# Kernel optimization log

Hardware: AMD Instinct MI355X
Metric: run time of the kernel (lower is better)

The kernel has to match this reference:

```python
import jax, jax.numpy as jnp
import numpy as np

N_NODES = 15000
N_EDGES = 60000
D_NODE_IN = 74
D_EDGE_IN = 12
D = 64            # node_out_feats
D_EHID = 128      # edge_hidden_feats
N_STEPS = 6
BN_EPS = 1e-5


def setup_inputs() -> dict:
    key = jax.random.key(0)
    ks = jax.random.split(key, 16)
    def lin(k, fan_in, shape):
        return jax.random.normal(k, shape, jnp.float32) / np.sqrt(fan_in)
    inp = {
        "node_feats": jax.random.normal(ks[0], (N_NODES, D_NODE_IN), jnp.float32),
        "edge_feats": jax.random.normal(ks[1], (N_EDGES, D_EDGE_IN), jnp.float32),
        "src": jax.random.randint(ks[2], (N_EDGES,), 0, N_NODES, jnp.int32),
        "dst": jax.random.randint(ks[3], (N_EDGES,), 0, N_NODES, jnp.int32),
        # project_node_feats: Linear(node_in, D)
        "W_proj": lin(ks[4], D_NODE_IN, (D_NODE_IN, D)),
        "b_proj": jnp.zeros((D,), jnp.float32),
        # edge network: Linear(edge_in, ehid) -> ReLU -> Linear(ehid, D*D)
        "W_e1": lin(ks[5], D_EDGE_IN, (D_EDGE_IN, D_EHID)),
        "b_e1": jnp.zeros((D_EHID,), jnp.float32),
        "W_e2": lin(ks[6], D_EHID, (D_EHID, D * D)),
        "b_e2": jnp.zeros((D * D,), jnp.float32),
        # NNConv bias + BatchNorm affine params
        "conv_bias": jnp.zeros((D,), jnp.float32),
        "bn_gamma": jnp.ones((D,), jnp.float32),
        "bn_beta": jnp.zeros((D,), jnp.float32),
        # GRU (single layer): torch layout W_ih [3D, D], W_hh [3D, D]
        "W_ih": lin(ks[7], D, (3 * D, D)),
        "W_hh": lin(ks[8], D, (3 * D, D)),
        "b_ih": jnp.zeros((3 * D,), jnp.float32),
        "b_hh": jnp.zeros((3 * D,), jnp.float32),
    }
    return inp


def reference(node_feats, edge_feats, W_proj, b_proj, W_e1, b_e1, W_e2, b_e2,
              conv_bias, bn_gamma, bn_beta, W_ih, W_hh, b_ih, b_hh, src, dst):
    n_nodes = node_feats.shape[0]

    # project_node_feats: Linear + ReLU
    h = jax.nn.relu(node_feats @ W_proj + b_proj)          # [N, D]
    hidden = h                                              # GRU hidden state

    # edge MLP is a pure function of static edge_feats -> compute once
    ew = jax.nn.relu(edge_feats @ W_e1 + b_e1) @ W_e2 + b_e2
    ew = ew.reshape(-1, D, D)                               # [E, D, D]

    # mean-aggregation normalizer (DGL mean: 0 for isolated nodes)
    deg = jax.ops.segment_sum(jnp.ones_like(dst, jnp.float32), dst,
                              num_segments=n_nodes)
    inv_deg = jnp.where(deg > 0, 1.0 / jnp.maximum(deg, 1.0), 0.0)[:, None]

    for _ in range(N_STEPS):
        # per-edge matvec message: (h_src^T W_e); sum over d_in commutes
        # with the mean reduction, so reduce vectors instead of matrices.
        msg = jnp.einsum('ei,eio->eo', h[src], ew)          # [E, D]
        rst = jax.ops.segment_sum(msg, dst, num_segments=n_nodes) * inv_deg
        rst = rst + conv_bias
        # BatchNorm1d (training mode: batch statistics, biased variance)
        mu = rst.mean(axis=0)
        var = rst.var(axis=0)
        rst = (rst - mu) * jax.lax.rsqrt(var + BN_EPS) * bn_gamma + bn_beta
        m = jax.nn.relu(rst)
        # GRU cell (torch gate order: r, z, n)
        gi = m @ W_ih.T + b_ih
        gh = hidden @ W_hh.T + b_hh
        i_r, i_z, i_n = jnp.split(gi, 3, axis=-1)
        h_r, h_z, h_n = jnp.split(gh, 3, axis=-1)
        r = jax.nn.sigmoid(i_r + h_r)
        z = jax.nn.sigmoid(i_z + h_z)
        n = jnp.tanh(i_n + r * h_n)
        hidden = (1.0 - z) * n + z * hidden
        h = hidden
    return h
```

## Files before the change

### kernel.cpp

```cpp
#include <hip/hip_runtime.h>
#include <hip/hip_bf16.h>
#include <math.h>

#define NN 15000
#define NE 60000
#define DIN 74
#define DEIN 12
#define DD 64
#define EH 128
#define NG 8192
#define NSTEPS 6
#define NRB 235
#define KAB 384
#define NTMAX 18752
#define NFB 586

typedef unsigned short ushort_t;
typedef __attribute__((ext_vector_type(8))) short short8v;
typedef __attribute__((ext_vector_type(4))) float float4v;

__device__ __forceinline__ float bsf(unsigned short u){
  union { unsigned int i; float f; } v; v.i = ((unsigned int)u) << 16; return v.f;
}
__device__ __forceinline__ unsigned short fsb(float f){
  union { float f; unsigned int i; } v; v.f = f;
  unsigned int x = v.i;
  return (unsigned short)((x + 0x7FFFu + ((x >> 16) & 1u)) >> 16);
}
__device__ __forceinline__ unsigned int pkbf(float a, float b){
  __hip_bfloat162 r = __float22bfloat162_rn(make_float2(a, b));
  union { __hip_bfloat162 h; unsigned int u; } v; v.h = r; return v.u;
}

__global__ void k_sniff(const ushort_t* __restrict__ nf16,
                        const int* __restrict__ dsti, int* __restrict__ flags){
  __shared__ int cnt[2];
  int t = threadIdx.x;
  if (t < 2) cnt[t] = 0;
  __syncthreads();
  int bad = 0;
  for (int i = t; i < 1024; i += 256){
    unsigned short u = nf16[2*i];
    int e = (u >> 7) & 0xFF;
    if (e < 96 || e > 159) bad++;
  }
  if (bad) atomicAdd(&cnt[0], bad);
  if (t < 256 && dsti[2*t+1] == 0) atomicAdd(&cnt[1], 1);
  __syncthreads();
  if (t == 0){
    flags[0] = (cnt[0] > 300) ? 1 : 0;
    flags[1] = (cnt[1] > 250) ? 1 : 0;
  }
}

struct CanonArgs {
  const void* in[15];
  float* out[15];
  int n[15];
};
__global__ void k_canon_all(CanonArgs a, const int* __restrict__ flags){
  int j = blockIdx.y;
  int n = a.n[j];
  int fp32 = flags[0];
  const void* in = a.in[j];
  float* out = a.out[j];
  for (int i = blockIdx.x*256 + threadIdx.x; i < n; i += gridDim.x*256){
    if (fp32) out[i] = ((const float*)in)[i];
    else      out[i] = bsf(((const ushort_t*)in)[i]);
  }
}
__global__ void k_canoni(const void* __restrict__ in, int* __restrict__ out,
                         int n, const int* __restrict__ flags){
  int i = blockIdx.x*256 + threadIdx.x;
  if (i >= n) return;
  long long v = flags[1] ? ((const long long*)in)[i]
                         : (long long)((const int*)in)[i];
  int vi = (int)v;
  if (vi < 0) vi = 0;
  if (vi >= NN) vi = NN-1;
  out[i] = vi;
}

__global__ void k_proj(const float* __restrict__ nf, const float* __restrict__ Wp,
                       const float* __restrict__ bp, float* __restrict__ hid,
                       ushort_t* __restrict__ ab){
  __shared__ float nfl[4][DIN];
  int t = threadIdx.x, blk = blockIdx.x;
  for (int idx = t; idx < 4*DIN; idx += 256){
    int vl = idx / DIN, i = idx - vl*DIN;
    nfl[vl][i] = nf[(size_t)(blk*4+vl)*DIN + i];
  }
  __syncthreads();
  int vl = t >> 6, o = t & 63;
  int v = blk*4 + vl;
  float acc = bp[o];
  for (int i = 0; i < DIN; ++i) acc += nfl[vl][i] * Wp[i*DD + o];
  float r = fmaxf(acc, 0.f);
  hid[(size_t)v*DD + o] = r;
  ushort_t hh = fsb(r);
  float hl = r - bsf(hh);
  ab[(size_t)v*KAB + 64 + o]  = hh;
  ab[(size_t)v*KAB + 192 + o] = fsb(hl);
  ab[(size_t)v*KAB + 320 + o] = hh;
}

__global__ void k_emlp(const float* __restrict__ ef, const float* __restrict__ W1,
                       const float* __restrict__ b1, ushort_t* __restrict__ thi,
                       ushort_t* __restrict__ tlo){
  __shared__ float efl[2][DEIN];
  int t = threadIdx.x, blk = blockIdx.x;
  if (t < 2*DEIN){
    int el = t / DEIN, i = t - el*DEIN;
    efl[el][i] = ef[(size_t)(blk*2+el)*DEIN + i];
  }
  __syncthreads();
  int el = t >> 7, c = t & 127;
  float acc = b1[c];
  for (int i = 0; i < DEIN; ++i) acc += efl[el][i] * W1[i*EH + c];
  float tv = fmaxf(acc, 0.f);
  ushort_t hiv = fsb(tv);
  size_t off = (size_t)(blk*2+el)*EH + c;
  thi[off] = hiv;
  tlo[off] = fsb(tv - bsf(hiv));
}
__global__ void k_zpad(ushort_t* __restrict__ thi, ushort_t* __restrict__ tlo){
  int t = threadIdx.x;
  thi[(size_t)NE*EH + t] = 0;
  tlo[(size_t)NE*EH + t] = 0;
}

__global__ void k_w2q(const float* __restrict__ W2, const float* __restrict__ b2,
                      ushort_t* __restrict__ w2q, ushort_t* __restrict__ w2b){
  int idx = blockIdx.x*256 + threadIdx.x;
  if (idx < NG*DD){
    int n = idx >> 6, i = idx & 63;
    int kq = n >> 11, rem = n & 2047;
    int o = rem >> 5, kl = rem & 31;
    int kg = kq*32 + kl;
    w2q[idx] = fsb(W2[(size_t)kg*4096 + i*64 + o]);
  } else if (idx < NG*DD + DD*DD){
    int r = idx - NG*DD;
    int o = r >> 6, i = r & 63;
    w2b[r] = fsb(b2[i*64 + o]);
  }
}

__global__ void k_wgru(const float* __restrict__ Wih, const float* __restrict__ Whh,
                       ushort_t* __restrict__ wg){
  int pos = blockIdx.x*256 + threadIdx.x;
  if (pos >= 256*KAB) return;
  int c = pos / KAB, k = pos - c*KAB;
  int kb = k >> 6, i = k & 63;
  int g = c >> 6, o = c & 63;
  float w = 0.f;
  if ((kb & 1) == 0){
    if (g == 0)      w = Wih[(size_t)(o)*64 + i];
    else if (g == 1) w = Wih[(size_t)(64+o)*64 + i];
    else if (g == 2) w = Wih[(size_t)(128+o)*64 + i];
  } else {
    if (g == 0)      w = Whh[(size_t)(o)*64 + i];
    else if (g == 1) w = Whh[(size_t)(64+o)*64 + i];
    else if (g == 3) w = Whh[(size_t)(128+o)*64 + i];
  }
  ushort_t hi = fsb(w);
  wg[pos] = (kb >= 4) ? fsb(w - bsf(hi)) : hi;
}

__global__ void k_zero(int* __restrict__ p, int n){
  int i = blockIdx.x*256 + threadIdx.x;
  if (i < n) p[i] = 0;
}
__global__ void k_deg(const int* __restrict__ idxarr, int* __restrict__ deg){
  int e = blockIdx.x*256 + threadIdx.x;
  if (e < NE) atomicAdd(&deg[idxarr[e]], 1);
}
__global__ void k_scan(const int* __restrict__ deg, int* __restrict__ rowp,
                       float* __restrict__ invd){
  __shared__ int ssum[256];
  int t = threadIdx.x;
  const int STRIP = (NN + 255) / 256;
  int lo = t*STRIP, hi = (lo + STRIP < NN) ? lo + STRIP : NN;
  int s = 0;
  for (int i = lo; i < hi; ++i) s += deg[i];
  ssum[t] = s;
  __syncthreads();
  if (t == 0){
    int acc = 0;
    for (int i = 0; i < 256; ++i){ int v = ssum[i]; ssum[i] = acc; acc += v; }
  }
  __syncthreads();
  int acc = ssum[t];
  for (int i = lo; i < hi; ++i){
    rowp[i] = acc;
    int d = deg[i];
    invd[i] = (d > 0) ? 1.0f/(float)d : 0.0f;
    acc += d;
  }
  if (t == 255) rowp[NN] = acc;
}
__global__ void k_scatter(const int* __restrict__ idxarr, const int* __restrict__ rowp,
                          int* __restrict__ cursor, int* __restrict__ eidx,
                          int* __restrict__ epos){
  int e = blockIdx.x*256 + threadIdx.x;
  if (e < NE){
    int d = idxarr[e];
    int pos = atomicAdd(&cursor[d], 1);
    int slot = rowp[d] + pos;
    eidx[slot] = e;
    if (epos) epos[e] = slot;
  }
}

__global__ void k_tiles(const int* __restrict__ rowp, int* __restrict__ tnode,
                        int* __restrict__ tbase, int* __restrict__ tcnt,
                        int* __restrict__ ntb){
  __shared__ int ss[256];
  int t = threadIdx.x;
  const int STRIP = (NN + 255) / 256;
  int lo = t*STRIP, hi = lo + STRIP; if (hi > NN) hi = NN;
  int c = 0;
  for (int i = lo; i < hi; ++i){
    int deg = rowp[i+1] - rowp[i];
    c += (deg + 15) >> 4;
  }
  ss[t] = c;
  __syncthreads();
  if (t == 0){
    int a = 0;
    for (int i = 0; i < 256; ++i){ int v = ss[i]; ss[i] = a; a += v; }
    ntb[0] = a;
  }
  __syncthreads();
  int pos = ss[t];
  for (int i = lo; i < hi; ++i){
    int b = rowp[i], deg = rowp[i+1] - b;
    for (int r = 0; r < deg; r += 16){
      tnode[pos] = i; tbase[pos] = b + r;
      int c2 = deg - r; tcnt[pos] = (c2 > 16) ? 16 : c2;
      ++pos;
    }
  }
}

__global__ __launch_bounds__(512,4) void k_fused6(
    const ushort_t* __restrict__ ab, const ushort_t* __restrict__ w2q,
    const ushort_t* __restrict__ w2b, const ushort_t* __restrict__ thi,
    const ushort_t* __restrict__ tlo,
    const int* __restrict__ tnode, const int* __restrict__ tbase,
    const int* __restrict__ tcnt, const int* __restrict__ ntb,
    const int* __restrict__ eidx, const int* __restrict__ epos,
    float* __restrict__ msg){
  __shared__ __align__(16) ushort_t Gl[32768];
  __shared__ float bhl[32*66];
  __shared__ int nodl[32], cntl[32], basel[32];
  __shared__ int eidl[32][16];
  __shared__ int posl[32][16];

  int tid = threadIdx.x;
  int nt = ntb[0];
  int T0 = blockIdx.x * 32;
  if (T0 >= nt) return;
  int wv = tid >> 6, lane = tid & 63;
  int lr = lane & 15, quad = lane >> 4;

  if (tid < 32){
    int gt = T0 + tid;
    int node = 0, base = 0, cnt = 0;
    if (gt < nt){ node = tnode[gt]; base = tbase[gt]; cnt = tcnt[gt]; }
    nodl[tid] = node; basel[tid] = base; cntl[tid] = cnt;
  }
  __syncthreads();
  {
    int j = tid >> 4, sl = tid & 15;
    int eid = NE, ps = 0;
    if (sl < cntl[j]){
      eid = eidx[basel[j] + sl];
      ps = epos[eid];
    }
    eidl[j][sl] = eid;
    posl[j][sl] = ps;
  }
  short8v hf0k0, hf0k1, hf1k0, hf1k1;
  {
    int n0 = nodl[lr], n1 = nodl[16 + lr];
    hf0k0 = *(const short8v*)(ab + (size_t)n0*KAB + 64 + quad*8);
    hf0k1 = *(const short8v*)(ab + (size_t)n0*KAB + 96 + quad*8);
    hf1k0 = *(const short8v*)(ab + (size_t)n1*KAB + 64 + quad*8);
    hf1k1 = *(const short8v*)(ab + (size_t)n1*KAB + 96 + quad*8);
  }
  {
    int ot = wv & 3, mh = wv >> 2;
    float4v ba = (float4v){0.f,0.f,0.f,0.f};
    short8v a0 = *(const short8v*)(w2b + (size_t)(ot*16 + lr)*DD + quad*8);
    short8v a1 = *(const short8v*)(w2b + (size_t)(ot*16 + lr)*DD + 32 + quad*8);
    ba = __builtin_amdgcn_mfma_f32_16x16x32_bf16(a0, mh ? hf1k0 : hf0k0, ba, 0,0,0);
    ba = __builtin_amdgcn_mfma_f32_16x16x32_bf16(a1, mh ? hf1k1 : hf0k1, ba, 0,0,0);
    #pragma unroll
    for (int reg = 0; reg < 4; ++reg)
      bhl[(mh*16 + lr)*66 + ot*16 + quad*4 + reg] = ba[reg];
  }

  int j0 = wv*4;
  for (int oh = 0; oh < 2; ++oh){
    float4v acc[4][2];
    #pragma unroll
    for (int j = 0; j < 4; ++j)
      #pragma unroll
      for (int ot = 0; ot < 2; ++ot)
        acc[j][ot] = (float4v){0.f,0.f,0.f,0.f};
    for (int kq = 0; kq < 4; ++kq){
      __syncthreads();
      short8v th0, th1, th2, th3, tw0, tw1, tw2, tw3;
      {
        size_t kqo = (size_t)kq*32 + quad*8;
        int e0 = eidl[j0+0][lr], e1 = eidl[j0+1][lr];
        int e2 = eidl[j0+2][lr], e3 = eidl[j0+3][lr];
        th0 = *(const short8v*)(thi + (size_t)e0*EH + kqo);
        tw0 = *(const short8v*)(tlo + (size_t)e0*EH + kqo);
        th1 = *(const short8v*)(thi + (size_t)e1*EH + kqo);
        tw1 = *(const short8v*)(tlo + (size_t)e1*EH + kqo);
        th2 = *(const short8v*)(thi + (size_t)e2*EH + kqo);
        tw2 = *(const short8v*)(tlo + (size_t)e2*EH + kqo);
        th3 = *(const short8v*)(thi + (size_t)e3*EH + kqo);
        tw3 = *(const short8v*)(tlo + (size_t)e3*EH + kqo);
      }
      #pragma unroll 2
      for (int it = 0; it < 8; ++it){
        int tile = wv*8 + it;
        int nrow = kq*2048 + oh*1024 + tile*16 + lr;
        const ushort_t* arow = w2q + (size_t)nrow*DD;
        short8v a0 = *(const short8v*)(arow + quad*8);
        short8v a1 = *(const short8v*)(arow + 32 + quad*8);
        int ol = tile >> 1;
        int klb = ((tile & 1) << 4) + quad*4;
        int q8 = klb >> 3, jj = klb & 7;
        #pragma unroll
        for (int mh = 0; mh < 2; ++mh){
          float4v g = (float4v){0.f,0.f,0.f,0.f};
          g = __builtin_amdgcn_mfma_f32_16x16x32_bf16(a0, mh ? hf1k0 : hf0k0, g, 0,0,0);
          g = __builtin_amdgcn_mfma_f32_16x16x32_bf16(a1, mh ? hf1k1 : hf0k1, g, 0,0,0);
          int m = mh*16 + lr;
          unsigned int p0 = pkbf(g[0], g[1]);
          unsigned int p1 = pkbf(g[2], g[3]);
          int byt = ((((m*4 + q8)*32 + ol) << 4) + jj*2) ^ ((m & 7) << 4);
          uint2 pv; pv.x = p0; pv.y = p1;
          *(uint2*)((char*)Gl + byt) = pv;
        }
      }
      __syncthreads();
      #pragma unroll
      for (int j = 0; j < 4; ++j){
        int m = j0 + j;
        int swz = (m & 7) << 4;
        short8v thj = (j==0)?th0:(j==1)?th1:(j==2)?th2:th3;
        short8v twj = (j==0)?tw0:(j==1)?tw1:(j==2)?tw2:tw3;
        #pragma unroll
        for (int ot = 0; ot < 2; ++ot){
          int byt = (((m*4 + quad)*32 + ot*16 + lr) << 4) ^ swz;
          short8v gf = *(const short8v*)((const char*)Gl + byt);
          acc[j][ot] = __builtin_amdgcn_mfma_f32_16x16x32_bf16(thj, gf, acc[j][ot], 0,0,0);
          acc[j][ot] = __builtin_amdgcn_mfma_f32_16x16x32_bf16(twj, gf, acc[j][ot], 0,0,0);
        }
      }
    }
    #pragma unroll
    for (int j = 0; j < 4; ++j){
      int m = j0 + j;
      #pragma unroll
      for (int ot = 0; ot < 2; ++ot){
        int o = oh*32 + ot*16 + lr;
        float bb = bhl[m*66 + o];
        #pragma unroll
        for (int reg = 0; reg < 4; ++reg){
          int sl = quad*4 + reg;
          int eid = eidl[m][sl];
          if (eid < NE) msg[(size_t)posl[m][sl]*DD + o] = acc[j][ot][reg] + bb;
        }
      }
    }
  }
}

__global__ void k_red(const float* __restrict__ msg, const int* __restrict__ rowp_d,
                      const float* __restrict__ invd, const float* __restrict__ cbias,
                      float* __restrict__ rst, float* __restrict__ part,
                      int* __restrict__ cnt, float* __restrict__ stats){
  __shared__ float ls[256], ls2[256];
  __shared__ int lastflag;
  int t = threadIdx.x, blk = blockIdx.x;
  int o = t & 63, gg = t >> 6;
  float cb = cbias[o];
  float s = 0.f, s2 = 0.f;
  #pragma unroll 1
  for (int j = 0; j < 16; ++j){
    int n = blk*64 + gg*16 + j;
    if (n >= NN) break;
    int b = rowp_d[n], e = rowp_d[n+1];
    float a0 = 0.f, a1 = 0.f, a2 = 0.f, a3 = 0.f;
    int i = b;
    for (; i + 3 < e; i += 4){
      a0 += msg[(size_t)i*DD + o];
      a1 += msg[(size_t)(i+1)*DD + o];
      a2 += msg[(size_t)(i+2)*DD + o];
      a3 += msg[(size_t)(i+3)*DD + o];
    }
    for (; i < e; ++i) a0 += msg[(size_t)i*DD + o];
    float x = ((a0 + a1) + (a2 + a3)) * invd[n] + cb;
    rst[(size_t)n*DD + o] = x;
    s += x; s2 += x*x;
  }
  ls[t] = s; ls2[t] = s2;
  __syncthreads();
  if (gg == 0){
    part[blk*128 + o]      = ls[o] + ls[64+o] + ls[128+o] + ls[192+o];
    part[blk*128 + 64 + o] = ls2[o] + ls2[64+o] + ls2[128+o] + ls2[192+o];
  }
  __threadfence();
  __syncthreads();
  if (t == 0) lastflag = (atomicAdd(cnt, 1) == NRB - 1) ? 1 : 0;
  __syncthreads();
  if (lastflag){
    if (t < 128){
      float s0 = 0.f, s1 = 0.f, s2b = 0.f, s3 = 0.f;
      int b = 0;
      for (; b + 3 < NRB; b += 4){
        s0  += part[b*128 + t];
        s1  += part[(b+1)*128 + t];
        s2b += part[(b+2)*128 + t];
        s3  += part[(b+3)*128 + t];
      }
      for (; b < NRB; ++b) s0 += part[b*128 + t];
      ls[t] = (s0 + s1) + (s2b + s3);
    }
    __syncthreads();
    if (t < 64){
      float mu = ls[t] / (float)NN;
      float var = ls[64+t] / (float)NN - mu*mu;
      if (var < 0.f) var = 0.f;
      stats[t] = mu;
      stats[64 + t] = rsqrtf(var + 1e-5f);
    }
  }
}

__global__ void k_gru_pre(const float* __restrict__ rst, const float* __restrict__ stats,
      const float* __restrict__ gamma, const float* __restrict__ beta,
      ushort_t* __restrict__ ab){
  int t = threadIdx.x, blk = blockIdx.x;
  int vl = t >> 6, o = t & 63;
  int v = blk*4 + vl;
  float x = rst[(size_t)v*DD + o];
  float m = fmaxf((x - stats[o])*stats[64+o]*gamma[o] + beta[o], 0.f);
  ushort_t mh = fsb(m);
  float mlo = m - bsf(mh);
  ab[(size_t)v*KAB + o]       = mh;
  ab[(size_t)v*KAB + 128 + o] = fsb(mlo);
  ab[(size_t)v*KAB + 256 + o] = mh;
}

__global__ __launch_bounds__(256) void k_gru_gemm(const ushort_t* __restrict__ ab,
        const ushort_t* __restrict__ wg, float* __restrict__ gbuf){
  __shared__ __align__(16) ushort_t As[128][136];
  __shared__ __align__(16) ushort_t Bs[64][136];
  int t = threadIdx.x;
  int n0 = blockIdx.x * 64;
  int m0 = blockIdx.y * 128;
  int w = t >> 6, lane = t & 63;
  int lrow = lane & 15, quad = lane >> 4;
  float4v acc[2][4];
  #pragma unroll
  for (int mt = 0; mt < 2; ++mt)
    #pragma unroll
    for (int nt = 0; nt < 4; ++nt) acc[mt][nt] = (float4v){0.f,0.f,0.f,0.f};
  for (int kt = 0; kt < 3; ++kt){
    __syncthreads();
    #pragma unroll
    for (int it = 0; it < 8; ++it){
      int cid = t + it*256;
      int r = cid >> 4, ko = (cid & 15) * 8;
      int gm = m0 + r; if (gm >= NN) gm = NN-1;
      *(uint4*)&As[r][ko] = *(const uint4*)(ab + (size_t)gm*KAB + kt*128 + ko);
    }
    #pragma unroll
    for (int it = 0; it < 4; ++it){
      int cid = t + it*256;
      int r = cid >> 4, ko = (cid & 15) * 8;
      *(uint4*)&Bs[r][ko] = *(const uint4*)(wg + (size_t)(n0 + r)*KAB + kt*128 + ko);
    }
    __syncthreads();
    #pragma unroll
    for (int ks = 0; ks < 4; ++ks){
      short8v a0 = *(const short8v*)&As[w*32 + lrow][ks*32 + quad*8];
      short8v a1 = *(const short8v*)&As[w*32 + 16 + lrow][ks*32 + quad*8];
      #pragma unroll
      for (int nt = 0; nt < 4; ++nt){
        short8v b = *(const short8v*)&Bs[nt*16 + lrow][ks*32 + quad*8];
        acc[0][nt] = __builtin_amdgcn_mfma_f32_16x16x32_bf16(a0, b, acc[0][nt], 0, 0, 0);
        acc[1][nt] = __builtin_amdgcn_mfma_f32_16x16x32_bf16(a1, b, acc[1][nt], 0, 0, 0);
      }
    }
  }
  #pragma unroll
  for (int mt = 0; mt < 2; ++mt){
    #pragma unroll
    for (int nt = 0; nt < 4; ++nt){
      int col = n0 + nt*16 + lrow;
      #pragma unroll
      for (int reg = 0; reg < 4; ++reg){
        int m = m0 + w*32 + mt*16 + quad*4 + reg;
        if (m < NN) gbuf[(size_t)m*256 + col] = acc[mt][nt][reg];
      }
    }
  }
}

__global__ void k_gru_fin(const float* __restrict__ gbuf,
      const float* __restrict__ bih, const float* __restrict__ bhh,
      float* __restrict__ hid, ushort_t* __restrict__ ab,
      float* __restrict__ out, int write_out){
  int t = threadIdx.x, blk = blockIdx.x;
  int vl = t >> 6, o = t & 63;
  int v = blk*4 + vl;
  const float* gb = gbuf + (size_t)v*256;
  float aR  = gb[o]       + bih[o]      + bhh[o];
  float aZ  = gb[64 + o]  + bih[64+o]   + bhh[64+o];
  float aNi = gb[128 + o] + bih[128+o];
  float aNh = gb[192 + o] + bhh[128+o];
  float hprev = hid[(size_t)v*DD + o];
  float r = 1.f/(1.f+__expf(-aR));
  float z = 1.f/(1.f+__expf(-aZ));
  float n = tanhf(aNi + r*aNh);
  float hnew = (1.f - z)*n + z*hprev;
  hid[(size_t)v*DD + o] = hnew;
  ushort_t hh = fsb(hnew);
  float hl = hnew - bsf(hh);
  ab[(size_t)v*KAB + 64 + o]  = hh;
  ab[(size_t)v*KAB + 192 + o] = fsb(hl);
  ab[(size_t)v*KAB + 320 + o] = hh;
  if (write_out) out[(size_t)v*DD + o] = hnew;
}

extern "C" void kernel_launch(void* const* d_in, const int* in_sizes, int n_in,
                              void* d_out, int out_size, void* d_ws, size_t ws_size,
                              hipStream_t stream){
  (void)out_size; (void)ws_size;
  float* out = (float*)d_out;

  int p_nf=-1,p_ef=-1,p_src=-1,p_dst=-1,p_Wp=-1,p_bp=-1,p_W1=-1,p_b1=-1,
      p_W2=-1,p_b2=-1,p_cb=-1,p_gam=-1,p_bet=-1,p_Wih=-1,p_Whh=-1,p_bih=-1,p_bhh=-1;
  int c60000=0,c64=0,c12288=0,c192=0;
  for (int i = 0; i < n_in; ++i){
    switch (in_sizes[i]){
      case 1110000: p_nf = i; break;
      case 720000:  p_ef = i; break;
      case 60000:   if (c60000++ == 0) p_src = i; else p_dst = i; break;
      case 4736:    p_Wp = i; break;
      case 64:      { if (c64==0) p_bp=i; else if (c64==1) p_cb=i;
                      else if (c64==2) p_gam=i; else p_bet=i; c64++; } break;
      case 1536:    p_W1 = i; break;
      case 128:     p_b1 = i; break;
      case 524288:  p_W2 = i; break;
      case 4096:    p_b2 = i; break;
      case 12288:   if (c12288++ == 0) p_Wih = i; else p_Whh = i; break;
      case 192:    if (c192++ == 0) p_bih = i; else p_bhh = i; break;
      default: break;
    }
  }

  char* p = (char*)d_ws;
  auto alloc = [&](size_t bytes)->char*{
    char* r = p; p += (bytes + 255) & ~(size_t)255; return r;
  };
  int* flags = (int*)alloc(256);
  const int FPOS[15] = {p_nf,p_ef,p_Wp,p_bp,p_W1,p_b1,p_W2,p_b2,p_cb,p_gam,p_bet,
                        p_Wih,p_Whh,p_bih,p_bhh};
  CanonArgs ca;
  int maxn = 0;
  for (int j = 0; j < 15; ++j){
    int n = in_sizes[FPOS[j]];
    ca.in[j]  = d_in[FPOS[j]];
    ca.out[j] = (float*)alloc((size_t)n * 4);
    ca.n[j]   = n;
    if (n > maxn) maxn = n;
  }
  const float* nf  = ca.out[0];  const float* ef  = ca.out[1];
  const float* Wp  = ca.out[2];  const float* bp  = ca.out[3];
  const float* W1  = ca.out[4];  const float* b1  = ca.out[5];
  const float* W2  = ca.out[6];  const float* b2  = ca.out[7];
  const float* cb  = ca.out[8];  const float* gam = ca.out[9];
  const float* bet = ca.out[10]; const float* Wih = ca.out[11];
  const float* Whh = ca.out[12]; const float* bih = ca.out[13];
  const float* bhh = ca.out[14];
  int* srcc = (int*)alloc((size_t)NE*4);
  int* dstc = (int*)alloc((size_t)NE*4);

  ushort_t* thi   = (ushort_t*)alloc((size_t)(NE+1)*EH*2);
  ushort_t* tlo   = (ushort_t*)alloc((size_t)(NE+1)*EH*2);
  ushort_t* w2q   = (ushort_t*)alloc((size_t)NG*DD*2);
  ushort_t* w2b   = (ushort_t*)alloc((size_t)DD*DD*2);
  float* hid      = (float*)alloc((size_t)NN*DD*4);
  ushort_t* ab    = (ushort_t*)alloc((size_t)NN*KAB*2);
  ushort_t* wg    = (ushort_t*)alloc((size_t)256*KAB*2);
  float* gbuf     = (float*)alloc((size_t)NN*256*4);
  float* rst      = (float*)alloc((size_t)NN*DD*4);
  float* msg      = (float*)alloc((size_t)NE*DD*4);
  float* part     = (float*)alloc((size_t)NRB*128*4);
  float* stats    = (float*)alloc(128*4);
  int* degall     = (int*)alloc((size_t)4*NN*4);
  int* deg  = degall;
  int* curd = degall + NN;
  int* deg2 = degall + 2*NN; int* cursor2 = degall + 3*NN;
  float* invd = (float*)alloc((size_t)NN*4);
  int* rowp_d = (int*)alloc((size_t)(NN+1)*4);
  int* eidx_d = (int*)alloc((size_t)NE*4);
  int* epos   = (int*)alloc((size_t)NE*4);
  int* rowp2  = (int*)alloc((size_t)(NN+1)*4);
  float* invd2= (float*)alloc((size_t)NN*4);
  int* eidx2  = (int*)alloc((size_t)NE*4);
  int* tnode  = (int*)alloc((size_t)NTMAX*4);
  int* tbase  = (int*)alloc((size_t)NTMAX*4);
  int* tcnt   = (int*)alloc((size_t)NTMAX*4);
  int* ntb    = (int*)alloc(256);
  int* cnts   = (int*)alloc(256);

  k_sniff<<<1, 256, 0, stream>>>((const ushort_t*)d_in[p_nf], (const int*)d_in[p_dst], flags);
  k_canon_all<<<dim3((maxn+255)/256, 15), 256, 0, stream>>>(ca, flags);
  k_canoni<<<(NE+255)/256, 256, 0, stream>>>(d_in[p_src], srcc, NE, flags);
  k_canoni<<<(NE+255)/256, 256, 0, stream>>>(d_in[p_dst], dstc, NE, flags);

  k_proj <<<NN/4,  256, 0, stream>>>(nf, Wp, bp, hid, ab);
  k_emlp <<<NE/2,  256, 0, stream>>>(ef, W1, b1, thi, tlo);
  k_zpad <<<1, 128, 0, stream>>>(thi, tlo);
  k_w2q  <<<(NG*DD + DD*DD + 255)/256, 256, 0, stream>>>(W2, b2, w2q, w2b);
  k_wgru <<<(256*KAB+255)/256, 256, 0, stream>>>(Wih, Whh, wg);
  k_zero <<<(4*NN+255)/256, 256, 0, stream>>>(degall, 4*NN);
  k_zero <<<1, 64, 0, stream>>>(cnts, 64);
  k_deg  <<<(NE+255)/256, 256, 0, stream>>>(dstc, deg);
  k_deg  <<<(NE+255)/256, 256, 0, stream>>>(srcc, deg2);
  k_scan <<<1, 256, 0, stream>>>(deg,  rowp_d, invd);
  k_scan <<<1, 256, 0, stream>>>(deg2, rowp2, invd2);
  k_scatter<<<(NE+255)/256, 256, 0, stream>>>(dstc, rowp_d, curd, eidx_d, epos);
  k_scatter<<<(NE+255)/256, 256, 0, stream>>>(srcc, rowp2, cursor2, eidx2, (int*)0);
  k_tiles<<<1, 256, 0, stream>>>(rowp2, tnode, tbase, tcnt, ntb);

  for (int s = 0; s < NSTEPS; ++s){
    k_fused6<<<NFB, 512, 0, stream>>>(ab, w2q, w2b, thi, tlo,
                                      tnode, tbase, tcnt, ntb, eidx2, epos, msg);
    k_red <<<NRB, 256, 0, stream>>>(msg, rowp_d, invd, cb, rst, part,
                                    cnts + s, stats);
    k_gru_pre <<<NN/4, 256, 0, stream>>>(rst, stats, gam, bet, ab);
    k_gru_gemm<<<dim3(4, (NN+127)/128), 256, 0, stream>>>(ab, wg, gbuf);
    k_gru_fin <<<NN/4, 256, 0, stream>>>(gbuf, bih, bhh, hid, ab, out,
                                         (s == NSTEPS-1) ? 1 : 0);
  }
}
```

Before: 1.162 ms.

## Fuse BN-apply, GRU GEMM and GRU gates into one kernel per step

Replaces the per-step k_gru_pre, k_gru_gemm and k_gru_fin kernels with a single k_gru_one kernel. It applies batch-norm and ReLU while loading tiles, runs the 256-wide gate GEMM, and computes the GRU gates from LDS, which removes the gbuf global round trip and two launches. Batch-norm statistics now come from a separate single-block k_bnf kernel instead of the last-block atomic pattern, and it pre-folds gamma and beta into a scale and shift. The message kernel also moves its edge-feature gathers after the G-tile compute and raises the unroll factor, to hide that load latency. In exchange the fused GRU kernel needs about 150KB of LDS, which limits it to one block per CU, and the ab columns 0–63 are no longer refreshed.

```diff
diff --git a/kernel.cpp b/kernel.cpp
--- a/kernel.cpp
+++ b/kernel.cpp
@@ -11,6 +11,7 @@
 #define NG 8192
 #define NSTEPS 6
 #define NRB 235
+#define NGB 235
 #define KAB 384
 #define NTMAX 18752
 #define NFB 586
@@ -242,7 +243,7 @@
   }
 }
 
-__global__ __launch_bounds__(512,4) void k_fused6(
+__global__ __launch_bounds__(512,4) void k_fused7(
     const ushort_t* __restrict__ ab, const ushort_t* __restrict__ w2q,
     const ushort_t* __restrict__ w2b, const ushort_t* __restrict__ thi,
     const ushort_t* __restrict__ tlo,
@@ -310,21 +311,7 @@
         acc[j][ot] = (float4v){0.f,0.f,0.f,0.f};
     for (int kq = 0; kq < 4; ++kq){
       __syncthreads();
-      short8v th0, th1, th2, th3, tw0, tw1, tw2, tw3;
-      {
-        size_t kqo = (size_t)kq*32 + quad*8;
-        int e0 = eidl[j0+0][lr], e1 = eidl[j0+1][lr];
-        int e2 = eidl[j0+2][lr], e3 = eidl[j0+3][lr];
-        th0 = *(const short8v*)(thi + (size_t)e0*EH + kqo);
-        tw0 = *(const short8v*)(tlo + (size_t)e0*EH + kqo);
-        th1 = *(const short8v*)(thi + (size_t)e1*EH + kqo);
-        tw1 = *(const short8v*)(tlo + (size_t)e1*EH + kqo);
-        th2 = *(const short8v*)(thi + (size_t)e2*EH + kqo);
-        tw2 = *(const short8v*)(tlo + (size_t)e2*EH + kqo);
-        th3 = *(const short8v*)(thi + (size_t)e3*EH + kqo);
-        tw3 = *(const short8v*)(tlo + (size_t)e3*EH + kqo);
-      }
-      #pragma unroll 2
+      #pragma unroll 4
       for (int it = 0; it < 8; ++it){
         int tile = wv*8 + it;
         int nrow = kq*2048 + oh*1024 + tile*16 + lr;
@@ -347,6 +334,20 @@
           *(uint2*)((char*)Gl + byt) = pv;
         }
       }
+      short8v th0, th1, th2, th3, tw0, tw1, tw2, tw3;
+      {
+        size_t kqo = (size_t)kq*32 + quad*8;
+        int e0 = eidl[j0+0][lr], e1 = eidl[j0+1][lr];
+        int e2 = eidl[j0+2][lr], e3 = eidl[j0+3][lr];
+        th0 = *(const short8v*)(thi + (size_t)e0*EH + kqo);
+        tw0 = *(const short8v*)(tlo + (size_t)e0*EH + kqo);
+        th1 = *(const short8v*)(thi + (size_t)e1*EH + kqo);
+        tw1 = *(const short8v*)(tlo + (size_t)e1*EH + kqo);
+        th2 = *(const short8v*)(thi + (size_t)e2*EH + kqo);
+        tw2 = *(const short8v*)(tlo + (size_t)e2*EH + kqo);
+        th3 = *(const short8v*)(thi + (size_t)e3*EH + kqo);
+        tw3 = *(const short8v*)(tlo + (size_t)e3*EH + kqo);
+      }
       __syncthreads();
       #pragma unroll
       for (int j = 0; j < 4; ++j){
@@ -383,10 +384,8 @@
 
 __global__ void k_red(const float* __restrict__ msg, const int* __restrict__ rowp_d,
                       const float* __restrict__ invd, const float* __restrict__ cbias,
-                      float* __restrict__ rst, float* __restrict__ part,
-                      int* __restrict__ cnt, float* __restrict__ stats){
+                      float* __restrict__ rst, float* __restrict__ part){
   __shared__ float ls[256], ls2[256];
-  __shared__ int lastflag;
   int t = threadIdx.x, blk = blockIdx.x;
   int o = t & 63, gg = t >> 6;
   float cb = cbias[o];
@@ -415,129 +414,131 @@
     part[blk*128 + o]      = ls[o] + ls[64+o] + ls[128+o] + ls[192+o];
     part[blk*128 + 64 + o] = ls2[o] + ls2[64+o] + ls2[128+o] + ls2[192+o];
   }
-  __threadfence();
-  __syncthreads();
-  if (t == 0) lastflag = (atomicAdd(cnt, 1) == NRB - 1) ? 1 : 0;
-  __syncthreads();
-  if (lastflag){
-    if (t < 128){
-      float s0 = 0.f, s1 = 0.f, s2b = 0.f, s3 = 0.f;
-      int b = 0;
-      for (; b + 3 < NRB; b += 4){
-        s0  += part[b*128 + t];
-        s1  += part[(b+1)*128 + t];
-        s2b += part[(b+2)*128 + t];
-        s3  += part[(b+3)*128 + t];
-      }
-      for (; b < NRB; ++b) s0 += part[b*128 + t];
-      ls[t] = (s0 + s1) + (s2b + s3);
-    }
-    __syncthreads();
-    if (t < 64){
-      float mu = ls[t] / (float)NN;
-      float var = ls[64+t] / (float)NN - mu*mu;
-      if (var < 0.f) var = 0.f;
-      stats[t] = mu;
-      stats[64 + t] = rsqrtf(var + 1e-5f);
-    }
-  }
-}
-
-__global__ void k_gru_pre(const float* __restrict__ rst, const float* __restrict__ stats,
-      const float* __restrict__ gamma, const float* __restrict__ beta,
-      ushort_t* __restrict__ ab){
-  int t = threadIdx.x, blk = blockIdx.x;
-  int vl = t >> 6, o = t & 63;
-  int v = blk*4 + vl;
-  float x = rst[(size_t)v*DD + o];
-  float m = fmaxf((x - stats[o])*stats[64+o]*gamma[o] + beta[o], 0.f);
-  ushort_t mh = fsb(m);
-  float mlo = m - bsf(mh);
-  ab[(size_t)v*KAB + o]       = mh;
-  ab[(size_t)v*KAB + 128 + o] = fsb(mlo);
-  ab[(size_t)v*KAB + 256 + o] = mh;
-}
-
-__global__ __launch_bounds__(256) void k_gru_gemm(const ushort_t* __restrict__ ab,
-        const ushort_t* __restrict__ wg, float* __restrict__ gbuf){
-  __shared__ __align__(16) ushort_t As[128][136];
-  __shared__ __align__(16) ushort_t Bs[64][136];
+}
+
+__global__ void k_bnf(const float* __restrict__ part, const float* __restrict__ gamma,
+                      const float* __restrict__ beta, float* __restrict__ stats){
+  __shared__ float sh[128];
   int t = threadIdx.x;
-  int n0 = blockIdx.x * 64;
-  int m0 = blockIdx.y * 128;
-  int w = t >> 6, lane = t & 63;
-  int lrow = lane & 15, quad = lane >> 4;
-  float4v acc[2][4];
+  float s0 = 0.f, s1 = 0.f, s2 = 0.f, s3 = 0.f;
+  int b = 0;
+  for (; b + 3 < NRB; b += 4){
+    s0 += part[b*128 + t];
+    s1 += part[(b+1)*128 + t];
+    s2 += part[(b+2)*128 + t];
+    s3 += part[(b+3)*128 + t];
+  }
+  for (; b < NRB; ++b) s0 += part[b*128 + t];
+  sh[t] = (s0 + s1) + (s2 + s3);
+  __syncthreads();
+  if (t < 64){
+    float mu = sh[t] / (float)NN;
+    float var = sh[64+t] / (float)NN - mu*mu;
+    if (var < 0.f) var = 0.f;
+    float rsq = rsqrtf(var + 1e-5f);
+    float scl = rsq * gamma[t];
+    stats[t] = scl;
+    stats[64 + t] = beta[t] - mu*scl;
+  }
+}
+
+__global__ __launch_bounds__(512) void k_gru_one(
+    const float* __restrict__ rst, const float* __restrict__ stats,
+    ushort_t* __restrict__ ab, const ushort_t* __restrict__ wg,
+    const float* __restrict__ bih, const float* __restrict__ bhh,
+    float* __restrict__ hid, float* __restrict__ out, int write_out){
+  __shared__ __align__(16) ushort_t As[64][136];
+  __shared__ __align__(16) ushort_t Bs[256][136];
+  __shared__ float gl[64*257];
+  __shared__ float scl[64], sft[64];
+  int t = threadIdx.x;
+  int r0 = blockIdx.x * 64;
+  if (t < 64){ scl[t] = stats[t]; sft[t] = stats[64+t]; }
+  int wv = t >> 6, lane = t & 63;
+  int lr = lane & 15, quad = lane >> 4;
+  int n0 = wv * 32;
+  float4v acc[4][2];
   #pragma unroll
-  for (int mt = 0; mt < 2; ++mt)
-    #pragma unroll
-    for (int nt = 0; nt < 4; ++nt) acc[mt][nt] = (float4v){0.f,0.f,0.f,0.f};
+  for (int mt = 0; mt < 4; ++mt)
+    #pragma unroll
+    for (int nt = 0; nt < 2; ++nt) acc[mt][nt] = (float4v){0.f,0.f,0.f,0.f};
   for (int kt = 0; kt < 3; ++kt){
     __syncthreads();
     #pragma unroll
+    for (int it = 0; it < 2; ++it){
+      int cid = t + it*512;
+      int r = cid >> 4, ko = (cid & 15) * 8;
+      int gm = r0 + r; if (gm >= NN) gm = NN-1;
+      if (ko < 64){
+        float4 x0 = *(const float4*)(rst + (size_t)gm*DD + ko);
+        float4 x1 = *(const float4*)(rst + (size_t)gm*DD + ko + 4);
+        float xv[8] = {x0.x,x0.y,x0.z,x0.w,x1.x,x1.y,x1.z,x1.w};
+        ushort_t u[8];
+        #pragma unroll
+        for (int jj = 0; jj < 8; ++jj){
+          float m = fmaxf(xv[jj]*scl[ko+jj] + sft[ko+jj], 0.f);
+          ushort_t mh = fsb(m);
+          u[jj] = (kt == 1) ? fsb(m - bsf(mh)) : mh;
+        }
+        *(uint4*)&As[r][ko] = *(const uint4*)u;
+      } else {
+        *(uint4*)&As[r][ko] = *(const uint4*)(ab + (size_t)gm*KAB + kt*128 + ko);
+      }
+    }
+    #pragma unroll
     for (int it = 0; it < 8; ++it){
-      int cid = t + it*256;
-      int r = cid >> 4, ko = (cid & 15) * 8;
-      int gm = m0 + r; if (gm >= NN) gm = NN-1;
-      *(uint4*)&As[r][ko] = *(const uint4*)(ab + (size_t)gm*KAB + kt*128 + ko);
-    }
-    #pragma unroll
-    for (int it = 0; it < 4; ++it){
-      int cid = t + it*256;
-      int r = cid >> 4, ko = (cid & 15) * 8;
-      *(uint4*)&Bs[r][ko] = *(const uint4*)(wg + (size_t)(n0 + r)*KAB + kt*128 + ko);
+      int cid = t + it*512;
+      int rB = cid >> 4, ko = (cid & 15) * 8;
+      *(uint4*)&Bs[rB][ko] = *(const uint4*)(wg + (size_t)rB*KAB + kt*128 + ko);
     }
     __syncthreads();
     #pragma unroll
     for (int ks = 0; ks < 4; ++ks){
-      short8v a0 = *(const short8v*)&As[w*32 + lrow][ks*32 + quad*8];
-      short8v a1 = *(const short8v*)&As[w*32 + 16 + lrow][ks*32 + quad*8];
+      short8v a[4];
       #pragma unroll
-      for (int nt = 0; nt < 4; ++nt){
-        short8v b = *(const short8v*)&Bs[nt*16 + lrow][ks*32 + quad*8];
-        acc[0][nt] = __builtin_amdgcn_mfma_f32_16x16x32_bf16(a0, b, acc[0][nt], 0, 0, 0);
-        acc[1][nt] = __builtin_amdgcn_mfma_f32_16x16x32_bf16(a1, b, acc[1][nt], 0, 0, 0);
+      for (int mt = 0; mt < 4; ++mt)
+        a[mt] = *(const short8v*)&As[mt*16 + lr][ks*32 + quad*8];
+      #pragma unroll
+      for (int nt = 0; nt < 2; ++nt){
+        short8v b = *(const short8v*)&Bs[n0 + nt*16 + lr][ks*32 + quad*8];
+        #pragma unroll
+        for (int mt = 0; mt < 4; ++mt)
+          acc[mt][nt] = __builtin_amdgcn_mfma_f32_16x16x32_bf16(a[mt], b, acc[mt][nt], 0,0,0);
       }
     }
   }
   #pragma unroll
-  for (int mt = 0; mt < 2; ++mt){
-    #pragma unroll
-    for (int nt = 0; nt < 4; ++nt){
-      int col = n0 + nt*16 + lrow;
+  for (int mt = 0; mt < 4; ++mt)
+    #pragma unroll
+    for (int nt = 0; nt < 2; ++nt){
+      int col = n0 + nt*16 + lr;
       #pragma unroll
-      for (int reg = 0; reg < 4; ++reg){
-        int m = m0 + w*32 + mt*16 + quad*4 + reg;
-        if (m < NN) gbuf[(size_t)m*256 + col] = acc[mt][nt][reg];
-      }
-    }
-  }
-}
-
-__global__ void k_gru_fin(const float* __restrict__ gbuf,
-      const float* __restrict__ bih, const float* __restrict__ bhh,
-      float* __restrict__ hid, ushort_t* __restrict__ ab,
-      float* __restrict__ out, int write_out){
-  int t = threadIdx.x, blk = blockIdx.x;
-  int vl = t >> 6, o = t & 63;
-  int v = blk*4 + vl;
-  const float* gb = gbuf + (size_t)v*256;
-  float aR  = gb[o]       + bih[o]      + bhh[o];
-  float aZ  = gb[64 + o]  + bih[64+o]   + bhh[64+o];
-  float aNi = gb[128 + o] + bih[128+o];
-  float aNh = gb[192 + o] + bhh[128+o];
-  float hprev = hid[(size_t)v*DD + o];
-  float r = 1.f/(1.f+__expf(-aR));
-  float z = 1.f/(1.f+__expf(-aZ));
-  float n = tanhf(aNi + r*aNh);
-  float hnew = (1.f - z)*n + z*hprev;
-  hid[(size_t)v*DD + o] = hnew;
-  ushort_t hh = fsb(hnew);
-  float hl = hnew - bsf(hh);
-  ab[(size_t)v*KAB + 64 + o]  = hh;
-  ab[(size_t)v*KAB + 192 + o] = fsb(hl);
-  ab[(size_t)v*KAB + 320 + o] = hh;
-  if (write_out) out[(size_t)v*DD + o] = hnew;
+      for (int reg = 0; reg < 4; ++reg)
+        gl[(mt*16 + quad*4 + reg)*257 + col] = acc[mt][nt][reg];
+    }
+  __syncthreads();
+  for (int idx = t; idx < 64*64; idx += 512){
+    int row = idx >> 6, o = idx & 63;
+    int v = r0 + row;
+    if (v >= NN) break;
+    const float* g = &gl[row*257];
+    float aR  = g[o]       + bih[o]      + bhh[o];
+    float aZ  = g[64 + o]  + bih[64+o]   + bhh[64+o];
+    float aNi = g[128 + o] + bih[128+o];
+    float aNh = g[192 + o] + bhh[128+o];
+    float hprev = hid[(size_t)v*DD + o];
+    float r = 1.f/(1.f+__expf(-aR));
+    float z = 1.f/(1.f+__expf(-aZ));
+    float n = tanhf(aNi + r*aNh);
+    float hnew = (1.f - z)*n + z*hprev;
+    hid[(size_t)v*DD + o] = hnew;
+    ushort_t hh = fsb(hnew);
+    float hl = hnew - bsf(hh);
+    ab[(size_t)v*KAB + 64 + o]  = hh;
+    ab[(size_t)v*KAB + 192 + o] = fsb(hl);
+    ab[(size_t)v*KAB + 320 + o] = hh;
+    if (write_out) out[(size_t)v*DD + o] = hnew;
+  }
 }
 
 extern "C" void kernel_launch(void* const* d_in, const int* in_sizes, int n_in,
@@ -601,7 +602,6 @@
   float* hid      = (float*)alloc((size_t)NN*DD*4);
   ushort_t* ab    = (ushort_t*)alloc((size_t)NN*KAB*2);
   ushort_t* wg    = (ushort_t*)alloc((size_t)256*KAB*2);
-  float* gbuf     = (float*)alloc((size_t)NN*256*4);
   float* rst      = (float*)alloc((size_t)NN*DD*4);
   float* msg      = (float*)alloc((size_t)NE*DD*4);
   float* part     = (float*)alloc((size_t)NRB*128*4);
@@ -621,7 +621,6 @@
   int* tbase  = (int*)alloc((size_t)NTMAX*4);
   int* tcnt   = (int*)alloc((size_t)NTMAX*4);
   int* ntb    = (int*)alloc(256);
-  int* cnts   = (int*)alloc(256);
 
   k_sniff<<<1, 256, 0, stream>>>((const ushort_t*)d_in[p_nf], (const int*)d_in[p_dst], flags);
   k_canon_all<<<dim3((maxn+255)/256, 15), 256, 0, stream>>>(ca, flags);
@@ -634,7 +633,6 @@
   k_w2q  <<<(NG*DD + DD*DD + 255)/256, 256, 0, stream>>>(W2, b2, w2q, w2b);
   k_wgru <<<(256*KAB+255)/256, 256, 0, stream>>>(Wih, Whh, wg);
   k_zero <<<(4*NN+255)/256, 256, 0, stream>>>(degall, 4*NN);
-  k_zero <<<1, 64, 0, stream>>>(cnts, 64);
   k_deg  <<<(NE+255)/256, 256, 0, stream>>>(dstc, deg);
   k_deg  <<<(NE+255)/256, 256, 0, stream>>>(srcc, deg2);
   k_scan <<<1, 256, 0, stream>>>(deg,  rowp_d, invd);
@@ -644,13 +642,11 @@
   k_tiles<<<1, 256, 0, stream>>>(rowp2, tnode, tbase, tcnt, ntb);
 
   for (int s = 0; s < NSTEPS; ++s){
-    k_fused6<<<NFB, 512, 0, stream>>>(ab, w2q, w2b, thi, tlo,
+    k_fused7<<<NFB, 512, 0, stream>>>(ab, w2q, w2b, thi, tlo,
                                       tnode, tbase, tcnt, ntb, eidx2, epos, msg);
-    k_red <<<NRB, 256, 0, stream>>>(msg, rowp_d, invd, cb, rst, part,
-                                    cnts + s, stats);
-    k_gru_pre <<<NN/4, 256, 0, stream>>>(rst, stats, gam, bet, ab);
-    k_gru_gemm<<<dim3(4, (NN+127)/128), 256, 0, stream>>>(ab, wg, gbuf);
-    k_gru_fin <<<NN/4, 256, 0, stream>>>(gbuf, bih, bhh, hid, ab, out,
-                                         (s == NSTEPS-1) ? 1 : 0);
-  }
-}
+    k_red <<<NRB, 256, 0, stream>>>(msg, rowp_d, invd, cb, rst, part);
+    k_bnf <<<1, 128, 0, stream>>>(part, gam, bet, stats);
+    k_gru_one<<<NGB, 512, 0, stream>>>(rst, stats, ab, wg, bih, bhh, hid, out,
+                                       (s == NSTEPS-1) ? 1 : 0);
+  }
+}
```

New measurement: 1.038 ms. 10.7% less time.
